# Kernel optimization log

Measured on AMD Instinct MI355X. Metric: run time of the kernel, lower is better.

## Reference

```python
import jax, jax.numpy as jnp
import numpy as np

N = 12288      # nodes
E = 393216     # edges (avg degree 32)
IN = 256       # in_feats
H = 128        # n_hidden
DZ = 64        # dim_z


def setup_inputs() -> dict:
    key = jax.random.key(0)
    k = jax.random.split(key, 6)
    features = jax.random.normal(k[0], (N, IN), dtype=jnp.float32)
    edge_index = jax.random.randint(k[1], (2, E), 0, N, dtype=jnp.int64)
    # torch init is uniform(-1/sqrt(out), 1/sqrt(out)); scaled normal is fine for a numeric baseline
    W0 = jax.random.normal(k[2], (IN, H), dtype=jnp.float32) / np.float32(np.sqrt(H))
    Wm = jax.random.normal(k[3], (H, DZ), dtype=jnp.float32) / np.float32(np.sqrt(DZ))
    Ws = jax.random.normal(k[4], (H, DZ), dtype=jnp.float32) / np.float32(np.sqrt(DZ))
    noise = jax.random.normal(k[5], (N, DZ), dtype=jnp.float32)
    return {"features": features, "W0": W0, "Wm": Wm, "Ws": Ws,
            "noise": noise, "edge_index": edge_index}


def reference(features, W0, Wm, Ws, noise, edge_index):
    src, dst = edge_index[0], edge_index[1]
    n = features.shape[0]
    # symmetric degree norm (in-degree), as stored in g.ndata['norm']
    deg = jax.ops.segment_sum(jnp.ones((src.shape[0],), features.dtype), dst, num_segments=n)
    norm = (1.0 / jnp.sqrt(jnp.clip(deg, 1.0)))[:, None]  # [N,1]

    def gcn_layer(h, W, act):
        h = (h @ W) * norm                                   # dense matmul + pre-norm
        h = jax.ops.segment_sum(h[src], dst, num_segments=n)  # copy_src -> sum aggregation
        h = h * norm                                          # post-norm
        return act(h) if act is not None else h

    hidden = gcn_layer(features, W0, None)
    mean = gcn_layer(hidden, Wm, jax.nn.relu)
    logstd = gcn_layer(hidden, Ws, jax.nn.relu)
    Z = noise * jnp.exp(logstd) + mean   # reparameterization
    adj_logits = Z @ Z.T                 # [N, N]
    return adj_logits
```

## Files before the change

### kernel.cpp

```cpp
#include <hip/hip_runtime.h>
#include <math.h>

#define Nn 12288
#define Ee 393216
#define INF 256
#define Hh 128
#define DZ 64

__global__ void deg_kernel(const int* __restrict__ dst, float* __restrict__ deg) {
    int i = blockIdx.x * 256 + threadIdx.x;
    if (i < Ee) atomicAdd(&deg[dst[i]], 1.0f);
}

__global__ __launch_bounds__(1024) void scan_kernel(const float* __restrict__ deg,
                                                    int* __restrict__ offs,
                                                    int* __restrict__ cursor,
                                                    float* __restrict__ nrm) {
    __shared__ int part[1024];
    int t = threadIdx.x;
    int base = t * 12;
    float dv[12];
    int loc[12];
    int s = 0;
#pragma unroll
    for (int k = 0; k < 12; ++k) {
        dv[k] = deg[base + k];
        loc[k] = s;
        s += (int)dv[k];
    }
    part[t] = s;
    __syncthreads();
    for (int off = 1; off < 1024; off <<= 1) {
        int v = (t >= off) ? part[t - off] : 0;
        __syncthreads();
        part[t] += v;
        __syncthreads();
    }
    int pre = (t == 0) ? 0 : part[t - 1];
#pragma unroll
    for (int k = 0; k < 12; ++k) {
        int o = pre + loc[k];
        offs[base + k] = o;
        cursor[base + k] = o;
        nrm[base + k] = 1.0f / sqrtf(fmaxf(dv[k], 1.0f));
    }
    if (t == 1023) offs[Nn] = part[1023];
}

__global__ void csr_kernel(const int* __restrict__ src, const int* __restrict__ dst,
                           int* __restrict__ cursor, int* __restrict__ csr_src) {
    int e = blockIdx.x * 256 + threadIdx.x;
    if (e < Ee) {
        int p = atomicAdd(&cursor[dst[e]], 1);
        csr_src[p] = src[e];
    }
}

__global__ __launch_bounds__(128) void gemm1_kernel(const float* __restrict__ X,
                                                    const float* __restrict__ W0,
                                                    const float* __restrict__ nrm,
                                                    float* __restrict__ out) {
    __shared__ float xs[16][INF];
    int r0 = blockIdx.x * 16;
    int tid = threadIdx.x;
    const float4* X4 = (const float4*)(X + (size_t)r0 * INF);
    float4* xs4 = (float4*)&xs[0][0];
    for (int idx = tid; idx < 16 * INF / 4; idx += 128) xs4[idx] = X4[idx];
    __syncthreads();
    int j = tid;
    float acc[16];
#pragma unroll
    for (int r = 0; r < 16; ++r) acc[r] = 0.0f;
    for (int k = 0; k < INF; ++k) {
        float w = W0[k * Hh + j];
#pragma unroll
        for (int r = 0; r < 16; ++r) acc[r] = fmaf(xs[r][k], w, acc[r]);
    }
#pragma unroll
    for (int r = 0; r < 16; ++r) out[(size_t)(r0 + r) * Hh + j] = acc[r] * nrm[r0 + r];
}

__global__ __launch_bounds__(128) void agg1_kernel(const int* __restrict__ csr_src,
                                                   const int* __restrict__ offs,
                                                   const float* __restrict__ tmp1,
                                                   float* __restrict__ agg1) {
    __shared__ int sidx[128];
    int node = blockIdx.x;
    int beg = offs[node], end = offs[node + 1];
    int f = threadIdx.x;
    float acc = 0.0f;
    for (int e0 = beg; e0 < end; e0 += 128) {
        int n = min(128, end - e0);
        if (f < n) sidx[f] = csr_src[e0 + f];
        __syncthreads();
        int t = 0;
        for (; t + 4 <= n; t += 4) {
            int s0 = sidx[t], s1 = sidx[t + 1], s2 = sidx[t + 2], s3 = sidx[t + 3];
            float v0 = tmp1[(size_t)s0 * Hh + f];
            float v1 = tmp1[(size_t)s1 * Hh + f];
            float v2 = tmp1[(size_t)s2 * Hh + f];
            float v3 = tmp1[(size_t)s3 * Hh + f];
            acc += (v0 + v1) + (v2 + v3);
        }
        for (; t < n; ++t) acc += tmp1[(size_t)sidx[t] * Hh + f];
        __syncthreads();
    }
    agg1[(size_t)node * Hh + f] = acc;
}

__global__ __launch_bounds__(128) void gemm2_kernel(const float* __restrict__ agg1,
                                                    const float* __restrict__ Wm,
                                                    const float* __restrict__ Ws,
                                                    const float* __restrict__ nrm_g,
                                                    float* __restrict__ outm,
                                                    float* __restrict__ outs) {
    __shared__ float hs[16][Hh];
    __shared__ float nl[16];
    int r0 = blockIdx.x * 16;
    int tid = threadIdx.x;
    if (tid < 16) nl[tid] = nrm_g[r0 + tid];
    __syncthreads();
    for (int idx = tid; idx < 16 * Hh / 4; idx += 128) {
        int row = idx >> 5;
        float4 v = ((const float4*)agg1)[(size_t)r0 * (Hh / 4) + idx];
        float s = nl[row];
        v.x *= s; v.y *= s; v.z *= s; v.w *= s;
        ((float4*)&hs[0][0])[idx] = v;
    }
    __syncthreads();
    int j = tid & 63, sel = tid >> 6;
    const float* W = sel ? Ws : Wm;
    float* out = sel ? outs : outm;
    float acc[16];
#pragma unroll
    for (int r = 0; r < 16; ++r) acc[r] = 0.0f;
    for (int k = 0; k < Hh; ++k) {
        float w = W[k * DZ + j];
#pragma unroll
        for (int r = 0; r < 16; ++r) acc[r] = fmaf(hs[r][k], w, acc[r]);
    }
#pragma unroll
    for (int r = 0; r < 16; ++r) out[(size_t)(r0 + r) * DZ + j] = acc[r] * nl[r];
}

__global__ __launch_bounds__(128) void agg2z_kernel(const int* __restrict__ csr_src,
                                                    const int* __restrict__ offs,
                                                    const float* __restrict__ tmpm,
                                                    const float* __restrict__ tmps,
                                                    const float* __restrict__ nrm,
                                                    const float* __restrict__ noise,
                                                    float* __restrict__ Z) {
    __shared__ int sidx[128];
    __shared__ float sbuf[64];
    int node = blockIdx.x;
    int beg = offs[node], end = offs[node + 1];
    int f = threadIdx.x & 63;
    const float* tin = (threadIdx.x >> 6) ? tmps : tmpm;
    float acc = 0.0f;
    for (int e0 = beg; e0 < end; e0 += 128) {
        int n = min(128, end - e0);
        if (threadIdx.x < n) sidx[threadIdx.x] = csr_src[e0 + threadIdx.x];
        __syncthreads();
        int t = 0;
        for (; t + 4 <= n; t += 4) {
            int s0 = sidx[t], s1 = sidx[t + 1], s2 = sidx[t + 2], s3 = sidx[t + 3];
            float v0 = tin[(size_t)s0 * DZ + f];
            float v1 = tin[(size_t)s1 * DZ + f];
            float v2 = tin[(size_t)s2 * DZ + f];
            float v3 = tin[(size_t)s3 * DZ + f];
            acc += (v0 + v1) + (v2 + v3);
        }
        for (; t < n; ++t) acc += tin[(size_t)sidx[t] * DZ + f];
        __syncthreads();
    }
    if (threadIdx.x >= 64) sbuf[f] = acc;
    __syncthreads();
    if (threadIdx.x < 64) {
        float nr = nrm[node];
        float m = fmaxf(acc * nr, 0.0f);
        float s = fmaxf(sbuf[f] * nr, 0.0f);
        size_t i = (size_t)node * DZ + f;
        Z[i] = fmaf(noise[i], expf(s), m);
    }
}

__global__ __launch_bounds__(256) void zzt_kernel(const float* __restrict__ Z,
                                                  float* __restrict__ out) {
    __shared__ float As[128 * 64];
    __shared__ float Bs[128 * 64];
    int i0 = blockIdx.y << 7, j0 = blockIdx.x << 7;
    int tid = threadIdx.x;

    for (int idx = tid; idx < 2048; idx += 256) {
        int row = idx >> 4;
        int c4 = idx & 15;
        int rot = (row >> 3) << 2;
        int cc = ((c4 << 2) + rot) & 63;
        float4 a = *(const float4*)(Z + ((size_t)(i0 + row) << 6) + (c4 << 2));
        float4 b = *(const float4*)(Z + ((size_t)(j0 + row) << 6) + (c4 << 2));
        *(float4*)&As[(row << 6) + cc] = a;
        *(float4*)&Bs[(row << 6) + cc] = b;
    }
    __syncthreads();

    int tx = tid & 15, ty = tid >> 4;
    float acc[8][8];
#pragma unroll
    for (int m = 0; m < 8; ++m)
#pragma unroll
        for (int n = 0; n < 8; ++n) acc[m][n] = 0.0f;

    int arot = ty << 2;
    int brot = tx << 2;
    const float* Abase = &As[(ty << 3) << 6];
    const float* Bbase = &Bs[(tx << 3) << 6];

#pragma unroll 2
    for (int k4 = 0; k4 < 16; ++k4) {
        int ka = ((k4 << 2) + arot) & 63;
        int kb = ((k4 << 2) + brot) & 63;
        float4 a4[8], b4[8];
#pragma unroll
        for (int m = 0; m < 8; ++m) a4[m] = *(const float4*)&Abase[(m << 6) + ka];
#pragma unroll
        for (int n = 0; n < 8; ++n) b4[n] = *(const float4*)&Bbase[(n << 6) + kb];
#pragma unroll
        for (int m = 0; m < 8; ++m)
#pragma unroll
            for (int n = 0; n < 8; ++n)
                acc[m][n] = fmaf(a4[m].w, b4[n].w,
                            fmaf(a4[m].z, b4[n].z,
                            fmaf(a4[m].y, b4[n].y,
                            fmaf(a4[m].x, b4[n].x, acc[m][n]))));
    }

#pragma unroll
    for (int m = 0; m < 8; ++m) {
        size_t row = (size_t)(i0 + (ty << 3) + m);
        float4 v0 = {acc[m][0], acc[m][1], acc[m][2], acc[m][3]};
        float4 v1 = {acc[m][4], acc[m][5], acc[m][6], acc[m][7]};
        *(float4*)(out + row * Nn + j0 + (tx << 3)) = v0;
        *(float4*)(out + row * Nn + j0 + (tx << 3) + 4) = v1;
    }
}

extern "C" void kernel_launch(void* const* d_in, const int* in_sizes, int n_in,
                              void* d_out, int out_size, void* d_ws, size_t ws_size,
                              hipStream_t stream) {
    const float* X = (const float*)d_in[0];
    const float* W0 = (const float*)d_in[1];
    const float* Wm = (const float*)d_in[2];
    const float* Ws = (const float*)d_in[3];
    const float* noise = (const float*)d_in[4];
    const int* ei = (const int*)d_in[5];
    const int* srcp = ei;
    const int* dstp = ei + Ee;
    float* out = (float*)d_out;

    float* ws = (float*)d_ws;
    float* deg  = ws;
    float* agg1 = deg + Nn;
    float* nrm  = agg1 + (size_t)Nn * Hh;
    float* tmp1 = nrm + Nn;
    float* tmpm = tmp1 + (size_t)Nn * Hh;
    float* tmps = tmpm + (size_t)Nn * DZ;
    float* Zb   = tmps + (size_t)Nn * DZ;
    int* offs    = (int*)(Zb + (size_t)Nn * DZ);
    int* cursor  = offs + Nn + 1;
    int* csr_src = cursor + Nn;

    hipMemsetAsync(deg, 0, (size_t)Nn * sizeof(float), stream);

    deg_kernel<<<(Ee + 255) / 256, 256, 0, stream>>>(dstp, deg);
    scan_kernel<<<1, 1024, 0, stream>>>(deg, offs, cursor, nrm);
    csr_kernel<<<(Ee + 255) / 256, 256, 0, stream>>>(srcp, dstp, cursor, csr_src);
    gemm1_kernel<<<Nn / 16, 128, 0, stream>>>(X, W0, nrm, tmp1);
    agg1_kernel<<<Nn, 128, 0, stream>>>(csr_src, offs, tmp1, agg1);
    gemm2_kernel<<<Nn / 16, 128, 0, stream>>>(agg1, Wm, Ws, nrm, tmpm, tmps);
    agg2z_kernel<<<Nn, 128, 0, stream>>>(csr_src, offs, tmpm, tmps, nrm, noise, Zb);
    dim3 g(Nn / 128, Nn / 128);
    zzt_kernel<<<g, 256, 0, stream>>>(Zb, out);
}
```

Measured before the change: 898.7 us.

## Compute Z·Zᵀ with split-bf16 MFMA instead of scalar FP32 FMA

```diff
diff --git a/kernel.cpp b/kernel.cpp
--- a/kernel.cpp
+++ b/kernel.cpp
@@ -6,6 +6,18 @@
 #define INF 256
 #define Hh 128
 #define DZ 64
+
+typedef short v8s __attribute__((ext_vector_type(8)));
+typedef float v4f __attribute__((ext_vector_type(4)));
+
+__device__ __forceinline__ unsigned short f2bf_rn(float f) {
+    unsigned int u = __float_as_uint(f);
+    unsigned int r = (u + 0x7FFFu + ((u >> 16) & 1u)) >> 16;
+    return (unsigned short)r;
+}
+__device__ __forceinline__ float bf2f(unsigned short h) {
+    return __uint_as_float((unsigned int)h << 16);
+}
 
 __global__ void deg_kernel(const int* __restrict__ dst, float* __restrict__ deg) {
     int i = blockIdx.x * 256 + threadIdx.x;
@@ -149,7 +161,8 @@
                                                     const float* __restrict__ tmps,
                                                     const float* __restrict__ nrm,
                                                     const float* __restrict__ noise,
-                                                    float* __restrict__ Z) {
+                                                    unsigned short* __restrict__ Zhi,
+                                                    unsigned short* __restrict__ Zlo) {
     __shared__ int sidx[128];
     __shared__ float sbuf[64];
     int node = blockIdx.x;
@@ -180,67 +193,69 @@
         float m = fmaxf(acc * nr, 0.0f);
         float s = fmaxf(sbuf[f] * nr, 0.0f);
         size_t i = (size_t)node * DZ + f;
-        Z[i] = fmaf(noise[i], expf(s), m);
-    }
-}
-
-__global__ __launch_bounds__(256) void zzt_kernel(const float* __restrict__ Z,
+        float z = fmaf(noise[i], expf(s), m);
+        unsigned short h = f2bf_rn(z);
+        Zhi[i] = h;
+        Zlo[i] = f2bf_rn(z - bf2f(h));
+    }
+}
+
+__global__ __launch_bounds__(256) void zzt_kernel(const unsigned short* __restrict__ Zhi,
+                                                  const unsigned short* __restrict__ Zlo,
                                                   float* __restrict__ out) {
-    __shared__ float As[128 * 64];
-    __shared__ float Bs[128 * 64];
     int i0 = blockIdx.y << 7, j0 = blockIdx.x << 7;
     int tid = threadIdx.x;
-
-    for (int idx = tid; idx < 2048; idx += 256) {
-        int row = idx >> 4;
-        int c4 = idx & 15;
-        int rot = (row >> 3) << 2;
-        int cc = ((c4 << 2) + rot) & 63;
-        float4 a = *(const float4*)(Z + ((size_t)(i0 + row) << 6) + (c4 << 2));
-        float4 b = *(const float4*)(Z + ((size_t)(j0 + row) << 6) + (c4 << 2));
-        *(float4*)&As[(row << 6) + cc] = a;
-        *(float4*)&Bs[(row << 6) + cc] = b;
-    }
-    __syncthreads();
-
-    int tx = tid & 15, ty = tid >> 4;
-    float acc[8][8];
-#pragma unroll
-    for (int m = 0; m < 8; ++m)
-#pragma unroll
-        for (int n = 0; n < 8; ++n) acc[m][n] = 0.0f;
-
-    int arot = ty << 2;
-    int brot = tx << 2;
-    const float* Abase = &As[(ty << 3) << 6];
-    const float* Bbase = &Bs[(tx << 3) << 6];
-
-#pragma unroll 2
-    for (int k4 = 0; k4 < 16; ++k4) {
-        int ka = ((k4 << 2) + arot) & 63;
-        int kb = ((k4 << 2) + brot) & 63;
-        float4 a4[8], b4[8];
-#pragma unroll
-        for (int m = 0; m < 8; ++m) a4[m] = *(const float4*)&Abase[(m << 6) + ka];
-#pragma unroll
-        for (int n = 0; n < 8; ++n) b4[n] = *(const float4*)&Bbase[(n << 6) + kb];
-#pragma unroll
-        for (int m = 0; m < 8; ++m)
-#pragma unroll
-            for (int n = 0; n < 8; ++n)
-                acc[m][n] = fmaf(a4[m].w, b4[n].w,
-                            fmaf(a4[m].z, b4[n].z,
-                            fmaf(a4[m].y, b4[n].y,
-                            fmaf(a4[m].x, b4[n].x, acc[m][n]))));
-    }
-
-#pragma unroll
-    for (int m = 0; m < 8; ++m) {
-        size_t row = (size_t)(i0 + (ty << 3) + m);
-        float4 v0 = {acc[m][0], acc[m][1], acc[m][2], acc[m][3]};
-        float4 v1 = {acc[m][4], acc[m][5], acc[m][6], acc[m][7]};
-        *(float4*)(out + row * Nn + j0 + (tx << 3)) = v0;
-        *(float4*)(out + row * Nn + j0 + (tx << 3) + 4) = v1;
+    int w = tid >> 6, lane = tid & 63;
+    int rsel = lane & 15;
+    int kgrp = (lane >> 4) << 3;
+
+    v4f acc[2][8];
+#pragma unroll
+    for (int mi = 0; mi < 2; ++mi)
+#pragma unroll
+        for (int nj = 0; nj < 8; ++nj) acc[mi][nj] = (v4f){0.f, 0.f, 0.f, 0.f};
+
+    int arow = i0 + (w << 5) + rsel;
+    int brow = j0 + rsel;
+
+#pragma unroll
+    for (int kh = 0; kh < 2; ++kh) {
+        int koff = (kh << 5) + kgrp;
+        v8s ahi[2], alo[2], bhi[8], blo[8];
+#pragma unroll
+        for (int mi = 0; mi < 2; ++mi) {
+            size_t p = (size_t)(arow + (mi << 4)) * DZ + koff;
+            ahi[mi] = *reinterpret_cast<const v8s*>(Zhi + p);
+            alo[mi] = *reinterpret_cast<const v8s*>(Zlo + p);
+        }
+#pragma unroll
+        for (int nj = 0; nj < 8; ++nj) {
+            size_t p = (size_t)(brow + (nj << 4)) * DZ + koff;
+            bhi[nj] = *reinterpret_cast<const v8s*>(Zhi + p);
+            blo[nj] = *reinterpret_cast<const v8s*>(Zlo + p);
+        }
+#pragma unroll
+        for (int mi = 0; mi < 2; ++mi)
+#pragma unroll
+            for (int nj = 0; nj < 8; ++nj) {
+                acc[mi][nj] = __builtin_amdgcn_mfma_f32_16x16x32_bf16(alo[mi], bhi[nj], acc[mi][nj], 0, 0, 0);
+                acc[mi][nj] = __builtin_amdgcn_mfma_f32_16x16x32_bf16(ahi[mi], blo[nj], acc[mi][nj], 0, 0, 0);
+                acc[mi][nj] = __builtin_amdgcn_mfma_f32_16x16x32_bf16(ahi[mi], bhi[nj], acc[mi][nj], 0, 0, 0);
+            }
+    }
+
+    int rowb = (lane >> 4) << 2;
+    int colb = lane & 15;
+#pragma unroll
+    for (int mi = 0; mi < 2; ++mi) {
+        int rbase = i0 + (w << 5) + (mi << 4) + rowb;
+#pragma unroll
+        for (int r = 0; r < 4; ++r) {
+            size_t rowoff = (size_t)(rbase + r) * Nn + j0 + colb;
+#pragma unroll
+            for (int nj = 0; nj < 8; ++nj)
+                out[rowoff + (nj << 4)] = acc[mi][nj][r];
+        }
     }
 }
 
@@ -264,8 +279,9 @@
     float* tmp1 = nrm + Nn;
     float* tmpm = tmp1 + (size_t)Nn * Hh;
     float* tmps = tmpm + (size_t)Nn * DZ;
-    float* Zb   = tmps + (size_t)Nn * DZ;
-    int* offs    = (int*)(Zb + (size_t)Nn * DZ);
+    unsigned short* Zhi = (unsigned short*)(tmps + (size_t)Nn * DZ);
+    unsigned short* Zlo = Zhi + (size_t)Nn * DZ;
+    int* offs    = (int*)(Zlo + (size_t)Nn * DZ);
     int* cursor  = offs + Nn + 1;
     int* csr_src = cursor + Nn;
 
@@ -277,7 +293,7 @@
     gemm1_kernel<<<Nn / 16, 128, 0, stream>>>(X, W0, nrm, tmp1);
     agg1_kernel<<<Nn, 128, 0, stream>>>(csr_src, offs, tmp1, agg1);
     gemm2_kernel<<<Nn / 16, 128, 0, stream>>>(agg1, Wm, Ws, nrm, tmpm, tmps);
-    agg2z_kernel<<<Nn, 128, 0, stream>>>(csr_src, offs, tmpm, tmps, nrm, noise, Zb);
+    agg2z_kernel<<<Nn, 128, 0, stream>>>(csr_src, offs, tmpm, tmps, nrm, noise, Zhi, Zlo);
     dim3 g(Nn / 128, Nn / 128);
-    zzt_kernel<<<g, 256, 0, stream>>>(Zb, out);
-}
+    zzt_kernel<<<g, 256, 0, stream>>>(Zhi, Zlo, out);
+}
```

Result: faster. 832.3 us (-7.4%).
